# Optimization experiments

Hardware: AMD Instinct MI355X
Metric: run time of the kernel (lower is better)

The kernel has to match this reference:

```python
import jax, jax.numpy as jnp
import numpy as np

B = 8192
D_IN = 10
H = 1900


def _l2norm_cols(w):
    # tf.nn.l2_normalize(w, dim=0): normalize each column, eps 1e-12
    sq = jnp.sum(w * w, axis=0, keepdims=True)
    return w * jax.lax.rsqrt(jnp.maximum(sq, 1e-12))


def setup_inputs() -> dict:
    key = jax.random.key(0)
    ks = jax.random.split(key, 12)
    return {
        "inputs": jax.random.normal(ks[0], (B, D_IN), jnp.float32),
        "c_prev": jax.random.normal(ks[1], (B, H), jnp.float32),
        "h_prev": jax.random.normal(ks[2], (B, H), jnp.float32),
        "wx": jax.random.normal(ks[3], (D_IN, 4 * H), jnp.float32) * 0.1,
        "wh": jax.random.normal(ks[4], (H, 4 * H), jnp.float32) * 0.1,
        "wmx": jax.random.normal(ks[5], (D_IN, H), jnp.float32) * 0.1,
        "wmh": jax.random.normal(ks[6], (H, H), jnp.float32) * 0.1,
        "b": jax.random.normal(ks[7], (4 * H,), jnp.float32) * 0.1,
        "gx": jax.random.uniform(ks[8], (4 * H,), jnp.float32, 0.5, 1.5),
        "gh": jax.random.uniform(ks[9], (4 * H,), jnp.float32, 0.5, 1.5),
        "gmx": jax.random.uniform(ks[10], (H,), jnp.float32, 0.5, 1.5),
        "gmh": jax.random.uniform(ks[11], (H,), jnp.float32, 0.5, 1.5),
    }


def reference(inputs, c_prev, h_prev, wx, wh, wmx, wmh, b, gx, gh, gmx, gmh):
    # weight-normalized weights (per-column l2 norm * gain)
    wx_n = _l2norm_cols(wx) * gx
    wh_n = _l2norm_cols(wh) * gh
    wmx_n = _l2norm_cols(wmx) * gmx
    wmh_n = _l2norm_cols(wmh) * gmh
    # multiplicative state m: [B, H]
    m = (inputs @ wmx_n) * (h_prev @ wmh_n)
    # gate pre-activations z: [B, 4H]
    z = inputs @ wx_n + m @ wh_n + b
    i, f, o, u = jnp.split(z, 4, axis=1)
    i = jax.nn.sigmoid(i)
    f = jax.nn.sigmoid(f)
    o = jax.nn.sigmoid(o)
    u = jnp.tanh(u)
    c = f * c_prev + i * u
    h = o * jnp.tanh(c)
    return (h, c)
```

## Files before the change

### kernel.cpp

```cpp
#include <hip/hip_runtime.h>

typedef unsigned short ushort_t;
typedef short bf16x8 __attribute__((ext_vector_type(8)));
typedef float f32x4 __attribute__((ext_vector_type(4)));

#define H 1900
#define FH 7600
#define BATCH 8192
#define KP 1952
#define NP_A 1920
#define NB 7680
#define BK 32
#define KITERS (KP / BK)

static const size_t OFF_SWX  = 0;
static const size_t OFF_SWH  = 32768;
static const size_t OFF_SWMX = 65536;
static const size_t OFF_SWMH = 73728;
static const size_t OFF_WMXN = 81920;
static const size_t OFF_PART = 163840;
static const size_t OFF_HBF  = 786432;
static const size_t OFF_MEXT = OFF_HBF + 31981568;
static const size_t OFF_WMHT = OFF_MEXT + 31981568;
static const size_t OFF_WHXT = OFF_WMHT + 7495680;

#define PW_X  0
#define PW_H  60800
#define PW_MX 121600
#define PW_MH 136800

__device__ __forceinline__ ushort_t f2bf(float x) {
  unsigned u = __float_as_uint(x);
  return (ushort_t)((u + 0x7fffu + ((u >> 16) & 1u)) >> 16);
}

__global__ void colsum_partial_kernel(const float* __restrict__ wx, const float* __restrict__ wh,
                                      const float* __restrict__ wmx, const float* __restrict__ wmh,
                                      float* __restrict__ parts) {
  int c = blockIdx.x * 256 + threadIdx.x;
  int y = blockIdx.y, p = blockIdx.z;
  const float* W; int K, N; float* out;
  if (y == 0)      { W = wx;  K = 10;   N = FH; out = parts + PW_X  + (size_t)p * FH; }
  else if (y == 1) { W = wh;  K = 1900; N = FH; out = parts + PW_H  + (size_t)p * FH; }
  else if (y == 2) { W = wmx; K = 10;   N = H;  out = parts + PW_MX + (size_t)p * H;  }
  else             { W = wmh; K = 1900; N = H;  out = parts + PW_MH + (size_t)p * H;  }
  if (c >= N) return;
  int rp = (K + 7) / 8;
  int r0 = p * rp, r1 = r0 + rp; if (r1 > K) r1 = K;
  float s = 0.f;
  for (int r = r0; r < r1; ++r) { float v = W[(size_t)r * N + c]; s += v * v; }
  out[c] = s;
}

__global__ void scales_final_kernel(const float* __restrict__ parts,
                                    const float* __restrict__ gx, const float* __restrict__ gh,
                                    const float* __restrict__ gmx, const float* __restrict__ gmh,
                                    float* __restrict__ s_wx, float* __restrict__ s_wh,
                                    float* __restrict__ s_wmx, float* __restrict__ s_wmh) {
  int c = blockIdx.x * 256 + threadIdx.x;
  int y = blockIdx.y;
  const float* pp; int N; const float* g; float* out;
  if (y == 0)      { pp = parts + PW_X;  N = FH; g = gx;  out = s_wx;  }
  else if (y == 1) { pp = parts + PW_H;  N = FH; g = gh;  out = s_wh;  }
  else if (y == 2) { pp = parts + PW_MX; N = H;  g = gmx; out = s_wmx; }
  else             { pp = parts + PW_MH; N = H;  g = gmh; out = s_wmh; }
  if (c >= N) return;
  float s = 0.f;
  for (int p = 0; p < 8; ++p) s += pp[(size_t)p * N + c];
  out[c] = g[c] * rsqrtf(fmaxf(s, 1e-12f));
}

__global__ void cvt_h_kernel(const float* __restrict__ h_prev, ushort_t* __restrict__ hbf) {
  size_t idx = (size_t)blockIdx.x * 256 + threadIdx.x;
  int row = (int)(idx / KP), col = (int)(idx % KP);
  float v = (col < H) ? h_prev[(size_t)row * H + col] : 0.f;
  hbf[idx] = f2bf(v);
}

__global__ void wmxn_kernel(const float* __restrict__ wmx, const float* __restrict__ s_wmx,
                            float* __restrict__ wmxn) {
  int idx = blockIdx.x * 256 + threadIdx.x;
  int i = idx / NP_A, j = idx - i * NP_A;
  wmxn[idx] = (j < H) ? wmx[i * H + j] * s_wmx[j] : 0.f;
}

__global__ void wmhT_kernel(const float* __restrict__ wmh, const float* __restrict__ s_wmh,
                            ushort_t* __restrict__ wmhT) {
  __shared__ float tile[32][33];
  int n0 = blockIdx.x * 32, k0 = blockIdx.y * 32;
  int tx = threadIdx.x & 31, ty = threadIdx.x >> 5;
#pragma unroll
  for (int it = 0; it < 4; ++it) {
    int k = k0 + ty + it * 8, n = n0 + tx;
    float v = (k < H && n < H) ? wmh[(size_t)k * H + n] : 0.f;
    tile[ty + it * 8][tx] = v;
  }
  __syncthreads();
#pragma unroll
  for (int it = 0; it < 4; ++it) {
    int n = n0 + ty + it * 8, k = k0 + tx;
    float v = tile[tx][ty + it * 8];
    float s = (n < H) ? s_wmh[n] : 0.f;
    wmhT[(size_t)n * KP + k] = f2bf(v * s);
  }
}

__global__ void whxT_kernel(const float* __restrict__ wh, const float* __restrict__ wx,
                            const float* __restrict__ s_wh, const float* __restrict__ s_wx,
                            ushort_t* __restrict__ whxT) {
  __shared__ float tile[32][33];
  int c0 = blockIdx.x * 32, k0 = blockIdx.y * 32;
  int tx = threadIdx.x & 31, ty = threadIdx.x >> 5;
#pragma unroll
  for (int it = 0; it < 4; ++it) {
    int k = k0 + ty + it * 8, c = c0 + tx;
    float v = 0.f;
    if (c < FH) {
      if (k < H) v = wh[(size_t)k * FH + c] * s_wh[c];
      else if (k >= NP_A && k < NP_A + 10) v = wx[(size_t)(k - NP_A) * FH + c] * s_wx[c];
    }
    tile[ty + it * 8][tx] = v;
  }
  __syncthreads();
#pragma unroll
  for (int it = 0; it < 4; ++it) {
    int c = c0 + ty + it * 8, k = k0 + tx;
    if (c < FH) {
      int g = c / H; int j = c - g * H; int n = 4 * j + g;
      whxT[(size_t)n * KP + k] = f2bf(tile[tx][ty + it * 8]);
    }
  }
}

__global__ void mext_tail_kernel(const float* __restrict__ inputs, ushort_t* __restrict__ m_ext) {
  int idx = blockIdx.x * 256 + threadIdx.x;
  int row = idx >> 5, c = idx & 31;
  float v = (c < 10) ? inputs[(size_t)row * 10 + c] : 0.f;
  m_ext[(size_t)row * KP + NP_A + c] = f2bf(v);
}

__global__ void whxT_tail_kernel(ushort_t* __restrict__ whxT) {
  int idx = blockIdx.x * 256 + threadIdx.x;
  whxT[(size_t)FH * KP + idx] = 0;
}

__device__ __forceinline__ void gemm_tile(const ushort_t* __restrict__ Ag,
                                          const ushort_t* __restrict__ Bg,
                                          int m0, int n0,
                                          ushort_t* As, ushort_t* Bs,
                                          f32x4 acc[4][4]) {
  const int tid = threadIdx.x;
  const int lane = tid & 63;
  const int quad = lane >> 4;
  const int lo = lane & 15;
  const int wave = tid >> 6;
  const int wm = (wave & 1) << 6;
  const int wn = (wave >> 1) << 6;
  const int sm = tid >> 1;
  const int sh = (tid & 1) << 4;
  const ushort_t* Ap = Ag + (size_t)(m0 + sm) * KP + sh;
  const ushort_t* Bp = Bg + (size_t)(n0 + sm) * KP + sh;
  for (int kt = 0; kt < KITERS; ++kt) {
    uint4 a0 = *(const uint4*)(Ap);
    uint4 a1 = *(const uint4*)(Ap + 8);
    uint4 b0 = *(const uint4*)(Bp);
    uint4 b1 = *(const uint4*)(Bp + 8);
    __syncthreads();
    *(uint4*)(As + sm * BK + sh)     = a0;
    *(uint4*)(As + sm * BK + sh + 8) = a1;
    *(uint4*)(Bs + sm * BK + sh)     = b0;
    *(uint4*)(Bs + sm * BK + sh + 8) = b1;
    __syncthreads();
    bf16x8 af[4], bfv[4];
#pragma unroll
    for (int mf = 0; mf < 4; ++mf)
      af[mf] = *(const bf16x8*)(As + (wm + mf * 16 + lo) * BK + quad * 8);
#pragma unroll
    for (int nf = 0; nf < 4; ++nf)
      bfv[nf] = *(const bf16x8*)(Bs + (wn + nf * 16 + lo) * BK + quad * 8);
#pragma unroll
    for (int mf = 0; mf < 4; ++mf)
#pragma unroll
      for (int nf = 0; nf < 4; ++nf)
        acc[mf][nf] = __builtin_amdgcn_mfma_f32_16x16x32_bf16(af[mf], bfv[nf], acc[mf][nf], 0, 0, 0);
    Ap += BK; Bp += BK;
  }
}

__global__ void __launch_bounds__(256) gemmA_kernel(const ushort_t* __restrict__ hbf,
                                                    const ushort_t* __restrict__ wmhT,
                                                    const float* __restrict__ inputs,
                                                    const float* __restrict__ wmxn,
                                                    ushort_t* __restrict__ m_ext) {
  __shared__ __align__(16) char smem[16384];
  ushort_t* As = (ushort_t*)smem;
  ushort_t* Bs = (ushort_t*)(smem + 8192);
  f32x4 acc[4][4];
  f32x4 zv = {0.f, 0.f, 0.f, 0.f};
#pragma unroll
  for (int a = 0; a < 4; ++a)
#pragma unroll
    for (int bq = 0; bq < 4; ++bq) acc[a][bq] = zv;
  int m0 = blockIdx.x * 128, n0 = blockIdx.y * 128;
  gemm_tile(hbf, wmhT, m0, n0, As, Bs, acc);
  __syncthreads();
  float* inL  = (float*)smem;
  float* wmxL = (float*)(smem + 5120);
  for (int t = threadIdx.x; t < 1280; t += 256) {
    int r = t / 10, i = t - r * 10;
    inL[t] = inputs[(size_t)(m0 + r) * 10 + i];
  }
  for (int t = threadIdx.x; t < 1280; t += 256) {
    int i = t >> 7, c = t & 127;
    wmxL[t] = wmxn[i * NP_A + n0 + c];
  }
  __syncthreads();
  const int lane = threadIdx.x & 63, quad = lane >> 4, lo = lane & 15;
  const int wave = threadIdx.x >> 6, wm = (wave & 1) << 6, wn = (wave >> 1) << 6;
#pragma unroll
  for (int mf = 0; mf < 4; ++mf)
#pragma unroll
    for (int r = 0; r < 4; ++r) {
      int rl = wm + mf * 16 + quad * 4 + r;
      float inrow[10];
#pragma unroll
      for (int i = 0; i < 10; ++i) inrow[i] = inL[rl * 10 + i];
#pragma unroll
      for (int nf = 0; nf < 4; ++nf) {
        int cl = wn + nf * 16 + lo;
        float mx = 0.f;
#pragma unroll
        for (int i = 0; i < 10; ++i) mx += inrow[i] * wmxL[i * 128 + cl];
        float mv = acc[mf][nf][r] * mx;
        m_ext[(size_t)(m0 + rl) * KP + (n0 + cl)] = f2bf(mv);
      }
    }
}

__global__ void __launch_bounds__(256) gemmB_kernel(const ushort_t* __restrict__ mext,
                                                    const ushort_t* __restrict__ whxT,
                                                    const float* __restrict__ bvec,
                                                    const float* __restrict__ c_prev,
                                                    float* __restrict__ hout,
                                                    float* __restrict__ cout) {
  __shared__ __align__(16) char smem[16384];
  ushort_t* As = (ushort_t*)smem;
  ushort_t* Bs = (ushort_t*)(smem + 8192);
  f32x4 acc[4][4];
  f32x4 zv = {0.f, 0.f, 0.f, 0.f};
#pragma unroll
  for (int a = 0; a < 4; ++a)
#pragma unroll
    for (int bq = 0; bq < 4; ++bq) acc[a][bq] = zv;
  int m0 = blockIdx.x * 128, n0 = blockIdx.y * 128;
  gemm_tile(mext, whxT, m0, n0, As, Bs, acc);
  const int lane = threadIdx.x & 63, quad = lane >> 4, lo = lane & 15;
  const int wave = threadIdx.x >> 6, wm = (wave & 1) << 6, wn = (wave >> 1) << 6;
#pragma unroll
  for (int nf = 0; nf < 4; ++nf) {
    int gn = n0 + wn + nf * 16 + lo;
    int j = gn >> 2, g = gn & 3;
    float bias = (j < H) ? bvec[g * H + j] : 0.f;
#pragma unroll
    for (int mf = 0; mf < 4; ++mf)
#pragma unroll
      for (int r = 0; r < 4; ++r) {
        float zs = acc[mf][nf][r] + bias;
        float v1 = __shfl_xor(zs, 1);
        float v2 = __shfl_xor(zs, 2);
        float v3 = __shfl_xor(v1, 2);
        if (g == r && j < H) {
          float zi, zf, zo, zu;
          { int t = 0 ^ g; zi = t == 0 ? zs : t == 1 ? v1 : t == 2 ? v2 : v3; }
          { int t = 1 ^ g; zf = t == 0 ? zs : t == 1 ? v1 : t == 2 ? v2 : v3; }
          { int t = 2 ^ g; zo = t == 0 ? zs : t == 1 ? v1 : t == 2 ? v2 : v3; }
          { int t = 3 ^ g; zu = t == 0 ? zs : t == 1 ? v1 : t == 2 ? v2 : v3; }
          float iv = 1.f / (1.f + __expf(-zi));
          float fv = 1.f / (1.f + __expf(-zf));
          float ov = 1.f / (1.f + __expf(-zo));
          float uv = tanhf(zu);
          int row = m0 + wm + mf * 16 + quad * 4 + r;
          size_t oidx = (size_t)row * H + j;
          float cp = c_prev[oidx];
          float cv = fv * cp + iv * uv;
          hout[oidx] = ov * tanhf(cv);
          cout[oidx] = cv;
        }
      }
  }
}

extern "C" void kernel_launch(void* const* d_in, const int* in_sizes, int n_in,
                              void* d_out, int out_size, void* d_ws, size_t ws_size,
                              hipStream_t stream) {
  const float* inputs = (const float*)d_in[0];
  const float* c_prev = (const float*)d_in[1];
  const float* h_prev = (const float*)d_in[2];
  const float* wx  = (const float*)d_in[3];
  const float* wh  = (const float*)d_in[4];
  const float* wmx = (const float*)d_in[5];
  const float* wmh = (const float*)d_in[6];
  const float* bv  = (const float*)d_in[7];
  const float* gx  = (const float*)d_in[8];
  const float* gh  = (const float*)d_in[9];
  const float* gmx = (const float*)d_in[10];
  const float* gmh = (const float*)d_in[11];

  char* ws = (char*)d_ws;
  float* s_wx  = (float*)(ws + OFF_SWX);
  float* s_wh  = (float*)(ws + OFF_SWH);
  float* s_wmx = (float*)(ws + OFF_SWMX);
  float* s_wmh = (float*)(ws + OFF_SWMH);
  float* wmxn  = (float*)(ws + OFF_WMXN);
  float* parts = (float*)(ws + OFF_PART);
  ushort_t* hbf   = (ushort_t*)(ws + OFF_HBF);
  ushort_t* m_ext = (ushort_t*)(ws + OFF_MEXT);
  ushort_t* wmhT  = (ushort_t*)(ws + OFF_WMHT);
  ushort_t* whxT  = (ushort_t*)(ws + OFF_WHXT);

  float* hout = (float*)d_out;
  float* cout = hout + (size_t)BATCH * H;

  colsum_partial_kernel<<<dim3(30, 4, 8), 256, 0, stream>>>(wx, wh, wmx, wmh, parts);
  scales_final_kernel<<<dim3(30, 4), 256, 0, stream>>>(parts, gx, gh, gmx, gmh,
                                                       s_wx, s_wh, s_wmx, s_wmh);
  cvt_h_kernel<<<62464, 256, 0, stream>>>(h_prev, hbf);
  wmxn_kernel<<<75, 256, 0, stream>>>(wmx, s_wmx, wmxn);
  wmhT_kernel<<<dim3(60, 61), 256, 0, stream>>>(wmh, s_wmh, wmhT);
  whxT_kernel<<<dim3(238, 61), 256, 0, stream>>>(wh, wx, s_wh, s_wx, whxT);
  mext_tail_kernel<<<1024, 256, 0, stream>>>(inputs, m_ext);
  whxT_tail_kernel<<<610, 256, 0, stream>>>(whxT);
  gemmA_kernel<<<dim3(64, 15), 256, 0, stream>>>(hbf, wmhT, inputs, wmxn, m_ext);
  gemmB_kernel<<<dim3(64, 60), 256, 0, stream>>>(m_ext, whxT, bv, c_prev, hout, cout);
}
```

Before: 1.097 ms.

## Load GEMM tiles directly into LDS and XOR-swizzle the shared layout

The shared GEMM tile loop now fills LDS with direct global-to-LDS loads instead of loading into registers and storing to shared memory. Each lane's 16-byte chunk is placed at an XOR-swizzled slot within its row, and the MFMA fragment reads apply the matching swizzle. This is meant to cut register pressure and staging instructions and to reduce LDS bank conflicts on fragment reads. The loads are now issued after the first barrier, so the global-load latency may be less hidden behind the previous iteration's work. The tile stays single-buffered.

```diff
diff --git a/kernel.cpp b/kernel.cpp
--- a/kernel.cpp
+++ b/kernel.cpp
@@ -32,6 +32,12 @@
 __device__ __forceinline__ ushort_t f2bf(float x) {
   unsigned u = __float_as_uint(x);
   return (ushort_t)((u + 0x7fffu + ((u >> 16) & 1u)) >> 16);
+}
+
+__device__ __forceinline__ void gl_lds16(const ushort_t* g, ushort_t* lds) {
+  __builtin_amdgcn_global_load_lds(
+      (const __attribute__((address_space(1))) unsigned int*)(g),
+      (__attribute__((address_space(3))) unsigned int*)(lds), 16, 0, 0);
 }
 
 __global__ void colsum_partial_kernel(const float* __restrict__ wx, const float* __restrict__ wh,
@@ -156,34 +162,41 @@
   const int wave = tid >> 6;
   const int wm = (wave & 1) << 6;
   const int wn = (wave >> 1) << 6;
-  const int sm = tid >> 1;
-  const int sh = (tid & 1) << 4;
-  const ushort_t* Ap = Ag + (size_t)(m0 + sm) * KP + sh;
-  const ushort_t* Bp = Bg + (size_t)(n0 + sm) * KP + sh;
+  const int sw = (lo >> 1) & 3;
+
+  const int cr = lane >> 2;
+  const int hg = (lane & 3) ^ ((lane >> 3) & 3);
+  const int r0 = wave * 16 + cr;
+  const int r1 = 64 + wave * 16 + cr;
+  const ushort_t* gA0 = Ag + (size_t)(m0 + r0) * KP + hg * 8;
+  const ushort_t* gA1 = Ag + (size_t)(m0 + r1) * KP + hg * 8;
+  const ushort_t* gB0 = Bg + (size_t)(n0 + r0) * KP + hg * 8;
+  const ushort_t* gB1 = Bg + (size_t)(n0 + r1) * KP + hg * 8;
+  ushort_t* lA0 = As + (wave * 16) * BK;
+  ushort_t* lA1 = As + (64 + wave * 16) * BK;
+  ushort_t* lB0 = Bs + (wave * 16) * BK;
+  ushort_t* lB1 = Bs + (64 + wave * 16) * BK;
+
   for (int kt = 0; kt < KITERS; ++kt) {
-    uint4 a0 = *(const uint4*)(Ap);
-    uint4 a1 = *(const uint4*)(Ap + 8);
-    uint4 b0 = *(const uint4*)(Bp);
-    uint4 b1 = *(const uint4*)(Bp + 8);
     __syncthreads();
-    *(uint4*)(As + sm * BK + sh)     = a0;
-    *(uint4*)(As + sm * BK + sh + 8) = a1;
-    *(uint4*)(Bs + sm * BK + sh)     = b0;
-    *(uint4*)(Bs + sm * BK + sh + 8) = b1;
+    gl_lds16(gA0, lA0);
+    gl_lds16(gA1, lA1);
+    gl_lds16(gB0, lB0);
+    gl_lds16(gB1, lB1);
     __syncthreads();
     bf16x8 af[4], bfv[4];
 #pragma unroll
     for (int mf = 0; mf < 4; ++mf)
-      af[mf] = *(const bf16x8*)(As + (wm + mf * 16 + lo) * BK + quad * 8);
+      af[mf] = *(const bf16x8*)(As + (wm + mf * 16 + lo) * BK + ((quad ^ sw) << 3));
 #pragma unroll
     for (int nf = 0; nf < 4; ++nf)
-      bfv[nf] = *(const bf16x8*)(Bs + (wn + nf * 16 + lo) * BK + quad * 8);
+      bfv[nf] = *(const bf16x8*)(Bs + (wn + nf * 16 + lo) * BK + ((quad ^ sw) << 3));
 #pragma unroll
     for (int mf = 0; mf < 4; ++mf)
 #pragma unroll
       for (int nf = 0; nf < 4; ++nf)
         acc[mf][nf] = __builtin_amdgcn_mfma_f32_16x16x32_bf16(af[mf], bfv[nf], acc[mf][nf], 0, 0, 0);
-    Ap += BK; Bp += BK;
+    gA0 += BK; gA1 += BK; gB0 += BK; gB1 += BK;
   }
 }
 
```

New measurement: 1.086 ms. Within noise of the previous version (-1.0%).
